# Optimization experiments

Hardware: AMD Instinct MI355X
Metric: run time of the kernel (lower is better)

The kernel has to match this reference:

```python
import jax, jax.numpy as jnp
import numpy as np

EMBED_DIM = 512
N_HEAD = 8
HEAD_DIM = EMBED_DIM // N_HEAD  # 64
B, S = 2, 4096
NEG_FILL = -1e20


def setup_inputs() -> dict:
    key = jax.random.key(0)
    ks = jax.random.split(key, 9)
    inp = {
        "key": jax.random.normal(ks[0], (B, S, EMBED_DIM), jnp.float32),
        "query": jax.random.normal(ks[1], (B, S, EMBED_DIM), jnp.float32),
        "value": jax.random.normal(ks[2], (B, S, EMBED_DIM), jnp.float32),
        "mask": jax.random.randint(ks[3], (1, 1, S, S), 0, 2, jnp.int32),
        # per-head projections (shared across heads, as in the source: a single
        # d x d nn.Linear applied to the last dim of [B,S,H,d])
        "Wq": jax.random.normal(ks[4], (HEAD_DIM, HEAD_DIM), jnp.float32) / np.sqrt(HEAD_DIM),
        "Wk": jax.random.normal(ks[5], (HEAD_DIM, HEAD_DIM), jnp.float32) / np.sqrt(HEAD_DIM),
        "Wv": jax.random.normal(ks[6], (HEAD_DIM, HEAD_DIM), jnp.float32) / np.sqrt(HEAD_DIM),
        "Wo": jax.random.normal(ks[7], (EMBED_DIM, EMBED_DIM), jnp.float32) / np.sqrt(EMBED_DIM),
        "bo": jax.random.normal(ks[8], (EMBED_DIM,), jnp.float32) * 0.01,
    }
    return inp


def reference(key, query, value, mask, Wq, Wk, Wv, Wo, bo):
    b, sq, e = query.shape
    skv = key.shape[1]
    h, d = N_HEAD, HEAD_DIM
    # split heads: [B, S, H, d]
    q = query.reshape(b, sq, h, d) @ Wq.T
    k = key.reshape(b, skv, h, d) @ Wk.T
    v = value.reshape(b, skv, h, d) @ Wv.T
    # scores: [B, H, Sq, Skv]
    scores = jnp.einsum("bqhd,bkhd->bhqk", q, k)
    # source masks BEFORE scaling: fill -1e20 then divide by sqrt(d)
    scores = jnp.where(mask == 0, NEG_FILL, scores)
    scores = scores / np.sqrt(d).astype(np.float32)
    attn = jax.nn.softmax(scores, axis=-1)
    ctx = jnp.einsum("bhqk,bkhd->bqhd", attn, v)  # [B, Sq, H, d]
    concat = ctx.reshape(b, sq, h * d)
    return concat @ Wo.T + bo
```

## Files before the change

### kernel.cpp

```cpp
#include <hip/hip_runtime.h>

typedef __bf16 bf16;
typedef __attribute__((ext_vector_type(8)))  bf16     bf16x8;
typedef __attribute__((ext_vector_type(4)))  bf16     bf16x4;
typedef __attribute__((ext_vector_type(16))) float    f32x16;
typedef __attribute__((ext_vector_type(4)))  float    f32x4;
typedef __attribute__((ext_vector_type(4)))  unsigned uint4v;
typedef __attribute__((ext_vector_type(2)))  unsigned uint2v;

#define SLEN 4096
#define HDIM 64
#define EMB 512
#define NTILES 64
#define SCALE_LOG2E 0.1803336100254854f

__device__ __forceinline__ f32x16 mfma32(bf16x8 a, bf16x8 b, f32x16 c) {
  return __builtin_amdgcn_mfma_f32_32x32x16_bf16(a, b, c, 0, 0, 0);
}

__device__ __forceinline__ void cp16(const void* g, const void* l) {
  __builtin_amdgcn_global_load_lds(
      (__attribute__((address_space(1))) unsigned int*)(unsigned long long)g,
      (__attribute__((address_space(3))) unsigned int*)(unsigned int)(unsigned long long)l,
      16, 0, 0);
}

__device__ __forceinline__ unsigned pk2(float a, float b) {
  unsigned short ua = __builtin_bit_cast(unsigned short, (bf16)a);
  unsigned short ub = __builtin_bit_cast(unsigned short, (bf16)b);
  return (unsigned)ua | ((unsigned)ub << 16);
}

__global__ __launch_bounds__(256, 2) void proj_qkv(
    const float* __restrict__ key, const float* __restrict__ query, const float* __restrict__ value,
    const float* __restrict__ Wq, const float* __restrict__ Wk, const float* __restrict__ Wv,
    bf16* __restrict__ Qb, bf16* __restrict__ Kb, bf16* __restrict__ VT)
{
  __shared__ __align__(16) bf16 tile[128][64];
  const int tid = threadIdx.x, w = tid >> 6, lane = tid & 63, l31 = lane & 31, lh = lane >> 5;
  const int r0 = blockIdx.x * 128;
  const int m0 = r0 + w * 32;

  #pragma unroll
  for (int p = 0; p < 3; ++p) {
    const float* X = (p == 0) ? query : (p == 1) ? key : value;
    const float* W = (p == 0) ? Wq    : (p == 1) ? Wk  : Wv;

    bf16x8 af[4];
    {
      const float* xr = X + (size_t)(m0 + l31) * 64 + 8 * lh;
      #pragma unroll
      for (int c = 0; c < 4; ++c) {
        f32x4 lo = *(const f32x4*)(xr + c * 16);
        f32x4 hi = *(const f32x4*)(xr + c * 16 + 4);
        bf16x8 v;
        #pragma unroll
        for (int j = 0; j < 4; ++j) { v[j] = (bf16)lo[j]; v[4 + j] = (bf16)hi[j]; }
        af[c] = v;
      }
    }
    bf16x8 bfr[2][4];
    #pragma unroll
    for (int nb = 0; nb < 2; ++nb) {
      const float* wr = W + (size_t)(l31 + 32 * nb) * 64 + 8 * lh;
      #pragma unroll
      for (int c = 0; c < 4; ++c) {
        f32x4 lo = *(const f32x4*)(wr + c * 16);
        f32x4 hi = *(const f32x4*)(wr + c * 16 + 4);
        bf16x8 v;
        #pragma unroll
        for (int j = 0; j < 4; ++j) { v[j] = (bf16)lo[j]; v[4 + j] = (bf16)hi[j]; }
        bfr[nb][c] = v;
      }
    }
    f32x16 a0, a1;
    #pragma unroll
    for (int r = 0; r < 16; ++r) { a0[r] = 0.f; a1[r] = 0.f; }
    #pragma unroll
    for (int c = 0; c < 4; ++c) {
      a0 = mfma32(af[c], bfr[0][c], a0);
      a1 = mfma32(af[c], bfr[1][c], a1);
    }

    const float qs = (p == 0) ? SCALE_LOG2E : 1.0f;
    __syncthreads();
    #pragma unroll
    for (int r = 0; r < 16; ++r) {
      const int row = w * 32 + (r & 3) + 8 * (r >> 2) + 4 * lh;
      tile[row][l31]      = (bf16)(a0[r] * qs);
      tile[row][l31 + 32] = (bf16)(a1[r] * qs);
    }
    __syncthreads();

    if (p < 2) {
      bf16* OUT = p ? Kb : Qb;
      const int rloc = tid >> 1, hf = tid & 1;
      const int rg = r0 + rloc, bs = rg >> 3, h = rg & 7, b = bs >> 12, sidx = bs & 4095;
      bf16* dst = OUT + (((size_t)(b * 8 + h) * SLEN + sidx) * 64 + hf * 32);
      const bf16* srcp = &tile[rloc][hf * 32];
      #pragma unroll
      for (int u = 0; u < 4; ++u) *(uint4v*)(dst + u * 8) = *(const uint4v*)(srcp + u * 8);
    } else {
      const int h = tid >> 5, d0 = tid & 31;
      const int b = blockIdx.x >> 8, s0 = (blockIdx.x * 16) & 4095;
      #pragma unroll
      for (int dh = 0; dh < 2; ++dh) {
        const int dd = d0 + 32 * dh;
        unsigned pk4[8];
        #pragma unroll
        for (int t2 = 0; t2 < 8; ++t2) {
          unsigned short ua = __builtin_bit_cast(unsigned short, tile[(2 * t2) * 8 + h][dd]);
          unsigned short ub = __builtin_bit_cast(unsigned short, tile[(2 * t2 + 1) * 8 + h][dd]);
          pk4[t2] = (unsigned)ua | ((unsigned)ub << 16);
        }
        bf16* dst = VT + ((size_t)(b * 8 + h) * 64 + dd) * SLEN + s0;
        uint4v A; A[0] = pk4[0]; A[1] = pk4[1]; A[2] = pk4[2]; A[3] = pk4[3];
        uint4v Bv; Bv[0] = pk4[4]; Bv[1] = pk4[5]; Bv[2] = pk4[6]; Bv[3] = pk4[7];
        *(uint4v*)(dst) = A;
        *(uint4v*)(dst + 8) = Bv;
      }
    }
  }
}

__device__ __forceinline__ unsigned nib_compress(unsigned x) {
  x = (x | (x >> 4)) & 0x00FF00FFu;
  x = (x | (x >> 8)) & 0x0000FFFFu;
  return x;
}
__global__ void pack_mask(const int* __restrict__ mask, unsigned* __restrict__ MW)
{
  const int w = threadIdx.x >> 6, lane = threadIdx.x & 63;
  const int q = blockIdx.x * 4 + w;
  const int* row = mask + (size_t)q * SLEN;
  unsigned long long mine = 0ull;
  #pragma unroll 4
  for (int i = 0; i < 64; ++i) {
    unsigned long long b = __ballot(row[i * 64 + lane] != 0);
    if (i == lane) mine = b;
  }
  const unsigned lo = (unsigned)mine, hi = (unsigned)(mine >> 32);
  const unsigned w0 = nib_compress(lo & 0x0F0F0F0Fu)        | (nib_compress(hi & 0x0F0F0F0Fu) << 16);
  const unsigned w1 = nib_compress((lo >> 4) & 0x0F0F0F0Fu) | (nib_compress((hi >> 4) & 0x0F0F0F0Fu) << 16);
  MW[(size_t)lane * SLEN + q] = w0;
  MW[(size_t)NTILES * SLEN + (size_t)lane * SLEN + q] = w1;
}

__global__ void wo_split(const float* __restrict__ Wo, bf16* __restrict__ WH, bf16* __restrict__ WL)
{
  const int i = (blockIdx.x * 256 + threadIdx.x) * 4;
  f32x4 v = *(const f32x4*)(Wo + i);
  bf16x4 h, l;
  #pragma unroll
  for (int j = 0; j < 4; ++j) { h[j] = (bf16)v[j]; l[j] = (bf16)(v[j] - (float)h[j]); }
  *(bf16x4*)(WH + i) = h;
  *(bf16x4*)(WL + i) = l;
}

__global__ __launch_bounds__(128, 4) void attn_kernel(
    const bf16* __restrict__ Qb, const bf16* __restrict__ Kb, const bf16* __restrict__ VT,
    const unsigned* __restrict__ MW,
    bf16* __restrict__ ctxh, bf16* __restrict__ ctxl)
{
  __shared__ __align__(16) unsigned char smem[16384];

  const int tid = threadIdx.x, w = tid >> 6, lane = tid & 63, l31 = lane & 31, lh = lane >> 5;
  const int logical = (blockIdx.x & 7) * 128 + (blockIdx.x >> 3);
  const int bh = logical >> 6, qt = logical & 63;
  const int q0w = qt * 64 + w * 32;
  const int qrow = q0w + l31;
  const int lh4 = 4 * lh;

  const bf16* qp = Qb + ((size_t)bh * SLEN + qrow) * HDIM + 8 * lh;
  const bf16x8 qf0 = *(const bf16x8*)(qp);
  const bf16x8 qf1 = *(const bf16x8*)(qp + 16);
  const bf16x8 qf2 = *(const bf16x8*)(qp + 32);
  const bf16x8 qf3 = *(const bf16x8*)(qp + 48);

  const bf16* kp0 = Kb + ((size_t)bh * SLEN + l31) * HDIM + (2 * w) * 16 + 8 * lh;
  const bf16* kp1 = kp0 + 16;
  const bf16* vp0 = VT + ((size_t)bh * HDIM + w * 32 + l31) * SLEN + 8 * lh;
  const bf16* vp1 = vp0 + 16;

  const int fk = 2 * w * 1024;
  const int fv = 4096 + 2 * w * 1024;
  const int lb = lane * 16;

  f32x16 o0, o1, Z16;
  #pragma unroll
  for (int r = 0; r < 16; ++r) { o0[r] = 0.f; o1[r] = 0.f; Z16[r] = 0.f; }
  float la0 = 0.f, la1 = 0.f, la2 = 0.f, la3 = 0.f;

#define STAGE(BUF) { \
  cp16(kp0, smem + (BUF) * 8192 + fk); cp16(kp1, smem + (BUF) * 8192 + fk + 1024); \
  cp16(vp0, smem + (BUF) * 8192 + fv); cp16(vp1, smem + (BUF) * 8192 + fv + 1024); \
  kp0 += 2048; kp1 += 2048; vp0 += 32; vp1 += 32; \
}

#define TILEC(BUF, MWORD, SH) { \
  const unsigned char* kr = smem + (BUF) * 8192 + lb; \
  __builtin_amdgcn_s_setprio(1); \
  f32x16 s = mfma32(*(const bf16x8*)(kr), qf0, Z16); \
  s = mfma32(*(const bf16x8*)(kr + 1024), qf1, s); \
  s = mfma32(*(const bf16x8*)(kr + 2048), qf2, s); \
  s = mfma32(*(const bf16x8*)(kr + 3072), qf3, s); \
  __builtin_amdgcn_s_setprio(0); \
  const unsigned mwk = (MWORD) >> (SH); \
  float p[16]; \
  _Pragma("unroll") \
  for (int r = 0; r < 16; ++r) { \
    float e = __builtin_amdgcn_exp2f(s[r]); \
    unsigned kbit = (unsigned)(((int)(mwk << (31 - r))) >> 31); \
    e = __builtin_bit_cast(float, __builtin_bit_cast(unsigned, e) & kbit); \
    p[r] = e; \
    if ((r & 3) == 0) la0 += e; else if ((r & 3) == 1) la1 += e; \
    else if ((r & 3) == 2) la2 += e; else la3 += e; \
  } \
  bf16x8 bp0, bp1; \
  { unsigned Wa = pk2(p[0], p[1]), Wb = pk2(p[2], p[3]); \
    unsigned Wc = pk2(p[4], p[5]), Wd = pk2(p[6], p[7]); \
    uint2v s02 = __builtin_amdgcn_permlane32_swap(Wa, Wc, false, false); \
    uint2v s13 = __builtin_amdgcn_permlane32_swap(Wb, Wd, false, false); \
    uint4v fw; fw[0] = s02[0]; fw[1] = s13[0]; fw[2] = s02[1]; fw[3] = s13[1]; \
    bp0 = __builtin_bit_cast(bf16x8, fw); } \
  { unsigned Wa = pk2(p[8], p[9]), Wb = pk2(p[10], p[11]); \
    unsigned Wc = pk2(p[12], p[13]), Wd = pk2(p[14], p[15]); \
    uint2v s02 = __builtin_amdgcn_permlane32_swap(Wa, Wc, false, false); \
    uint2v s13 = __builtin_amdgcn_permlane32_swap(Wb, Wd, false, false); \
    uint4v fw; fw[0] = s02[0]; fw[1] = s13[0]; fw[2] = s02[1]; fw[3] = s13[1]; \
    bp1 = __builtin_bit_cast(bf16x8, fw); } \
  const unsigned char* vr = kr + 4096; \
  __builtin_amdgcn_s_setprio(1); \
  o0 = mfma32(*(const bf16x8*)(vr), bp0, o0); \
  o0 = mfma32(*(const bf16x8*)(vr + 1024), bp1, o0); \
  o1 = mfma32(*(const bf16x8*)(vr + 2048), bp0, o1); \
  o1 = mfma32(*(const bf16x8*)(vr + 3072), bp1, o1); \
  __builtin_amdgcn_s_setprio(0); \
}

#define SYNC_STAGED \
  asm volatile("s_waitcnt vmcnt(4)" ::: "memory"); \
  __builtin_amdgcn_sched_barrier(0); \
  __builtin_amdgcn_s_barrier(); \
  __builtin_amdgcn_sched_barrier(0);

#define SYNC_READ_DONE \
  __builtin_amdgcn_sched_barrier(0); \
  __builtin_amdgcn_s_barrier(); \
  __builtin_amdgcn_sched_barrier(0);

  const unsigned* mp = MW + (size_t)lh * NTILES * SLEN + qrow;

  STAGE(0)
  unsigned mwc = *mp;

  for (int t2 = 0; t2 < 64; ++t2) {
    STAGE(1)
    SYNC_STAGED
    const unsigned mwn = mp[(t2 < 63) ? SLEN : 0];
    TILEC(0, mwc, 0)
    SYNC_READ_DONE

    STAGE(0)
    SYNC_STAGED
    TILEC(1, mwc, 16)
    SYNC_READ_DONE

    mwc = mwn; mp += SLEN;
  }
#undef STAGE
#undef TILEC
#undef SYNC_STAGED
#undef SYNC_READ_DONE

  asm volatile("s_waitcnt vmcnt(0)" ::: "memory");
  __builtin_amdgcn_s_barrier();

  float plsum = (la0 + la1) + (la2 + la3);
  plsum += __shfl_xor(plsum, 32);
  const float inv = 1.f / plsum;
  #pragma unroll
  for (int r = 0; r < 16; ++r) { o0[r] *= inv; o1[r] *= inv; }

  bf16* T = (bf16*)(smem + w * 8192);
  const int qq = lane >> 1, hf = lane & 1;
  bf16* dsth = ctxh + ((size_t)bh * SLEN + q0w + qq) * 64 + hf * 32;
  bf16* dstl = ctxl + ((size_t)bh * SLEN + q0w + qq) * 64 + hf * 32;
  const bf16* sp = T + qq * 72 + hf * 32;

  #pragma unroll
  for (int r = 0; r < 16; ++r) {
    const int dr = (r & 3) + 8 * (r >> 2) + lh4;
    T[l31 * 72 + dr]      = (bf16)o0[r];
    T[l31 * 72 + 32 + dr] = (bf16)o1[r];
  }
  #pragma unroll
  for (int u = 0; u < 4; ++u) *(uint4v*)(dsth + u * 8) = *(const uint4v*)(sp + u * 8);
  #pragma unroll
  for (int r = 0; r < 16; ++r) {
    const int dr = (r & 3) + 8 * (r >> 2) + lh4;
    const float h0 = (float)(bf16)o0[r];
    const float h1 = (float)(bf16)o1[r];
    T[l31 * 72 + dr]      = (bf16)(o0[r] - h0);
    T[l31 * 72 + 32 + dr] = (bf16)(o1[r] - h1);
  }
  #pragma unroll
  for (int u = 0; u < 4; ++u) *(uint4v*)(dstl + u * 8) = *(const uint4v*)(sp + u * 8);
}

__global__ __launch_bounds__(256, 2) void out_proj(
    const bf16* __restrict__ CH, const bf16* __restrict__ CL,
    const bf16* __restrict__ WH, const bf16* __restrict__ WL,
    const float* __restrict__ bo, float* __restrict__ out)
{
  __shared__ __align__(16) bf16 Af[2][4][4][64][8];
  const int tid = threadIdx.x, w = tid >> 6, lane = tid & 63, l31 = lane & 31, lh = lane >> 5;
  const int mt = blockIdx.x >> 3, nt = blockIdx.x & 7;
  const int bs0 = mt * 128, n0 = nt * 64;
  const int b = bs0 >> 12, sbase = bs0 & 4095;

  f32x16 a0, a1;
  #pragma unroll
  for (int r = 0; r < 16; ++r) { a0[r] = 0.f; a1[r] = 0.f; }

  for (int kk = 0; kk < 8; ++kk) {
    __syncthreads();
    #pragma unroll
    for (int qq = 0; qq < 8; ++qq) {
      const int fid = w * 8 + qq, pl = fid >> 4, mb = (fid >> 2) & 3, c = fid & 3;
      const bf16* src = (pl ? CL : CH) +
          ((size_t)(b * 8 + kk) * SLEN + sbase + 32 * mb + l31) * 64 + 16 * c + 8 * lh;
      cp16(src, &Af[pl][mb][c][0][0]);
    }
    __syncthreads();

    bf16x8 bh0[4], bl0[4], bh1[4], bl1[4], ah[4], al[4];
    #pragma unroll
    for (int c = 0; c < 4; ++c) {
      const size_t o0off = (size_t)(n0 + l31) * EMB + kk * 64 + 16 * c + 8 * lh;
      const size_t o1off = (size_t)(n0 + l31 + 32) * EMB + kk * 64 + 16 * c + 8 * lh;
      bh0[c] = *(const bf16x8*)(WH + o0off);
      bl0[c] = *(const bf16x8*)(WL + o0off);
      bh1[c] = *(const bf16x8*)(WH + o1off);
      bl1[c] = *(const bf16x8*)(WL + o1off);
      ah[c] = *(const bf16x8*)(&Af[0][w][c][lane][0]);
      al[c] = *(const bf16x8*)(&Af[1][w][c][lane][0]);
    }
    #pragma unroll
    for (int c = 0; c < 4; ++c) {
      a0 = mfma32(ah[c], bh0[c], a0);
      a0 = mfma32(ah[c], bl0[c], a0);
      a0 = mfma32(al[c], bh0[c], a0);
      a1 = mfma32(ah[c], bh1[c], a1);
      a1 = mfma32(ah[c], bl1[c], a1);
      a1 = mfma32(al[c], bh1[c], a1);
    }
  }

  const float bv0 = bo[n0 + l31], bv1 = bo[n0 + l31 + 32];
  #pragma unroll
  for (int r = 0; r < 16; ++r) {
    const int row = bs0 + w * 32 + (r & 3) + 8 * (r >> 2) + 4 * lh;
    out[(size_t)row * EMB + n0 + l31]      = a0[r] + bv0;
    out[(size_t)row * EMB + n0 + l31 + 32] = a1[r] + bv1;
  }
}

extern "C" void kernel_launch(void* const* d_in, const int* in_sizes, int n_in,
                              void* d_out, int out_size, void* d_ws, size_t ws_size,
                              hipStream_t stream)
{
  (void)in_sizes; (void)n_in; (void)out_size; (void)ws_size;
  const float* key   = (const float*)d_in[0];
  const float* query = (const float*)d_in[1];
  const float* value = (const float*)d_in[2];
  const int*   mask  = (const int*)d_in[3];
  const float* Wq    = (const float*)d_in[4];
  const float* Wk    = (const float*)d_in[5];
  const float* Wv    = (const float*)d_in[6];
  const float* Wo    = (const float*)d_in[7];
  const float* bo    = (const float*)d_in[8];
  float* out = (float*)d_out;

  char* ws = (char*)d_ws;
  bf16* Qb = (bf16*)(ws);
  bf16* Kb = (bf16*)(ws + (8ull  << 20));
  bf16* VT = (bf16*)(ws + (16ull << 20));
  unsigned* MW = (unsigned*)(ws + (24ull << 20));
  bf16* CH = (bf16*)(ws + (26ull << 20));
  bf16* CL = (bf16*)(ws + (34ull << 20));
  bf16* WH = (bf16*)(ws + (42ull << 20));
  bf16* WL = (bf16*)(ws + (42ull << 20) + (512ull << 10));

  proj_qkv<<<512, 256, 0, stream>>>(key, query, value, Wq, Wk, Wv, Qb, Kb, VT);
  pack_mask<<<1024, 256, 0, stream>>>(mask, MW);
  wo_split<<<256, 256, 0, stream>>>(Wo, WH, WL);
  attn_kernel<<<1024, 128, 0, stream>>>(Qb, Kb, VT, MW, CH, CL);
  out_proj<<<512, 256, 0, stream>>>(CH, CL, WH, WL, bo, out);
}
```

Before: 237.0 us.

## Split attention KV range into two halves and combine partial outputs

```diff
diff --git a/kernel.cpp b/kernel.cpp
--- a/kernel.cpp
+++ b/kernel.cpp
@@ -160,16 +160,16 @@
 __global__ __launch_bounds__(128, 4) void attn_kernel(
     const bf16* __restrict__ Qb, const bf16* __restrict__ Kb, const bf16* __restrict__ VT,
     const unsigned* __restrict__ MW,
-    bf16* __restrict__ ctxh, bf16* __restrict__ ctxl)
+    float* __restrict__ PO, float* __restrict__ PLg)
 {
   __shared__ __align__(16) unsigned char smem[16384];
 
   const int tid = threadIdx.x, w = tid >> 6, lane = tid & 63, l31 = lane & 31, lh = lane >> 5;
-  const int logical = (blockIdx.x & 7) * 128 + (blockIdx.x >> 3);
-  const int bh = logical >> 6, qt = logical & 63;
+  const int logical = (blockIdx.x & 7) * 256 + (blockIdx.x >> 3);
+  const int qt = logical & 63, bh = (logical >> 6) & 15, half = logical >> 10;
   const int q0w = qt * 64 + w * 32;
   const int qrow = q0w + l31;
-  const int lh4 = 4 * lh;
+  const int kv0 = half * 2048;
 
   const bf16* qp = Qb + ((size_t)bh * SLEN + qrow) * HDIM + 8 * lh;
   const bf16x8 qf0 = *(const bf16x8*)(qp);
@@ -177,9 +177,9 @@
   const bf16x8 qf2 = *(const bf16x8*)(qp + 32);
   const bf16x8 qf3 = *(const bf16x8*)(qp + 48);
 
-  const bf16* kp0 = Kb + ((size_t)bh * SLEN + l31) * HDIM + (2 * w) * 16 + 8 * lh;
+  const bf16* kp0 = Kb + ((size_t)bh * SLEN + kv0 + l31) * HDIM + (2 * w) * 16 + 8 * lh;
   const bf16* kp1 = kp0 + 16;
-  const bf16* vp0 = VT + ((size_t)bh * HDIM + w * 32 + l31) * SLEN + 8 * lh;
+  const bf16* vp0 = VT + ((size_t)bh * HDIM + w * 32 + l31) * SLEN + kv0 + 8 * lh;
   const bf16* vp1 = vp0 + 16;
 
   const int fk = 2 * w * 1024;
@@ -249,15 +249,15 @@
   __builtin_amdgcn_s_barrier(); \
   __builtin_amdgcn_sched_barrier(0);
 
-  const unsigned* mp = MW + (size_t)lh * NTILES * SLEN + qrow;
+  const unsigned* mp = MW + (size_t)lh * NTILES * SLEN + (size_t)(half * 32) * SLEN + qrow;
 
   STAGE(0)
   unsigned mwc = *mp;
 
-  for (int t2 = 0; t2 < 64; ++t2) {
+  for (int t2 = 0; t2 < 32; ++t2) {
     STAGE(1)
     SYNC_STAGED
-    const unsigned mwn = mp[(t2 < 63) ? SLEN : 0];
+    const unsigned mwn = mp[(t2 < 31) ? SLEN : 0];
     TILEC(0, mwc, 0)
     SYNC_READ_DONE
 
@@ -278,34 +278,66 @@
 
   float plsum = (la0 + la1) + (la2 + la3);
   plsum += __shfl_xor(plsum, 32);
-  const float inv = 1.f / plsum;
-  #pragma unroll
-  for (int r = 0; r < 16; ++r) { o0[r] *= inv; o1[r] *= inv; }
-
-  bf16* T = (bf16*)(smem + w * 8192);
-  const int qq = lane >> 1, hf = lane & 1;
-  bf16* dsth = ctxh + ((size_t)bh * SLEN + q0w + qq) * 64 + hf * 32;
-  bf16* dstl = ctxl + ((size_t)bh * SLEN + q0w + qq) * 64 + hf * 32;
-  const bf16* sp = T + qq * 72 + hf * 32;
+
+  float* T = (float*)(smem + w * 8192);
+  const int qq = lane >> 1, hx = lane & 1;
+  float* dst = PO + ((size_t)((half * 16 + bh) * SLEN + q0w + qq)) * 64 + hx * 16;
+  const float* sp = T + qq * 33 + hx * 16;
 
   #pragma unroll
   for (int r = 0; r < 16; ++r) {
-    const int dr = (r & 3) + 8 * (r >> 2) + lh4;
-    T[l31 * 72 + dr]      = (bf16)o0[r];
-    T[l31 * 72 + 32 + dr] = (bf16)o1[r];
-  }
-  #pragma unroll
-  for (int u = 0; u < 4; ++u) *(uint4v*)(dsth + u * 8) = *(const uint4v*)(sp + u * 8);
+    const int dr = (r & 3) + 8 * (r >> 2) + 4 * lh;
+    T[l31 * 33 + dr] = o0[r];
+  }
+  #pragma unroll
+  for (int u = 0; u < 4; ++u) *(f32x4*)(dst + u * 4) = *(const f32x4*)(sp + u * 4);
   #pragma unroll
   for (int r = 0; r < 16; ++r) {
-    const int dr = (r & 3) + 8 * (r >> 2) + lh4;
-    const float h0 = (float)(bf16)o0[r];
-    const float h1 = (float)(bf16)o1[r];
-    T[l31 * 72 + dr]      = (bf16)(o0[r] - h0);
-    T[l31 * 72 + 32 + dr] = (bf16)(o1[r] - h1);
-  }
-  #pragma unroll
-  for (int u = 0; u < 4; ++u) *(uint4v*)(dstl + u * 8) = *(const uint4v*)(sp + u * 8);
+    const int dr = (r & 3) + 8 * (r >> 2) + 4 * lh;
+    T[l31 * 33 + dr] = o1[r];
+  }
+  #pragma unroll
+  for (int u = 0; u < 4; ++u) *(f32x4*)(dst + 32 + u * 4) = *(const f32x4*)(sp + u * 4);
+
+  if (lane < 32) PLg[(size_t)(half * 16 + bh) * SLEN + q0w + l31] = plsum;
+}
+
+__global__ __launch_bounds__(256) void combine_halves(
+    const float* __restrict__ PO, const float* __restrict__ PLg,
+    bf16* __restrict__ CH, bf16* __restrict__ CL)
+{
+  const int bh = blockIdx.x >> 5, qt = blockIdx.x & 31;
+  const int t = threadIdx.x;
+  const int q = qt * 128 + (t >> 1);
+  const size_t HOFF = (size_t)16 * SLEN * 64;
+  const size_t base = ((size_t)bh * SLEN + q) * 64 + (t & 1) * 32;
+  const float inv = 1.f / (PLg[(size_t)bh * SLEN + q] +
+                           PLg[(size_t)16 * SLEN + (size_t)bh * SLEN + q]);
+  const float* p0 = PO + base;
+  const float* p1 = PO + HOFF + base;
+  unsigned hw[16], lw[16];
+  #pragma unroll
+  for (int i = 0; i < 8; ++i) {
+    f32x4 a = *(const f32x4*)(p0 + i * 4);
+    f32x4 b = *(const f32x4*)(p1 + i * 4);
+    float v0 = (a[0] + b[0]) * inv, v1 = (a[1] + b[1]) * inv;
+    float v2 = (a[2] + b[2]) * inv, v3 = (a[3] + b[3]) * inv;
+    float h0 = (float)(bf16)v0, h1 = (float)(bf16)v1;
+    float h2 = (float)(bf16)v2, h3 = (float)(bf16)v3;
+    hw[i * 2]     = pk2(v0, v1);
+    hw[i * 2 + 1] = pk2(v2, v3);
+    lw[i * 2]     = pk2(v0 - h0, v1 - h1);
+    lw[i * 2 + 1] = pk2(v2 - h2, v3 - h3);
+  }
+  bf16* ch = CH + base;
+  bf16* cl = CL + base;
+  #pragma unroll
+  for (int u = 0; u < 4; ++u) {
+    uint4v H; H[0] = hw[u*4]; H[1] = hw[u*4+1]; H[2] = hw[u*4+2]; H[3] = hw[u*4+3];
+    uint4v L; L[0] = lw[u*4]; L[1] = lw[u*4+1]; L[2] = lw[u*4+2]; L[3] = lw[u*4+3];
+    *(uint4v*)(ch + u * 8) = H;
+    *(uint4v*)(cl + u * 8) = L;
+  }
 }
 
 __global__ __launch_bounds__(256, 2) void out_proj(
@@ -391,10 +423,13 @@
   bf16* CL = (bf16*)(ws + (34ull << 20));
   bf16* WH = (bf16*)(ws + (42ull << 20));
   bf16* WL = (bf16*)(ws + (42ull << 20) + (512ull << 10));
+  float* PO  = (float*)(ws + (44ull << 20));
+  float* PLg = (float*)(ws + (78ull << 20));
 
   proj_qkv<<<512, 256, 0, stream>>>(key, query, value, Wq, Wk, Wv, Qb, Kb, VT);
   pack_mask<<<1024, 256, 0, stream>>>(mask, MW);
   wo_split<<<256, 256, 0, stream>>>(Wo, WH, WL);
-  attn_kernel<<<1024, 128, 0, stream>>>(Qb, Kb, VT, MW, CH, CL);
+  attn_kernel<<<2048, 128, 0, stream>>>(Qb, Kb, VT, MW, PO, PLg);
+  combine_halves<<<512, 256, 0, stream>>>(PO, PLg, CH, CL);
   out_proj<<<512, 256, 0, stream>>>(CH, CL, WH, WL, bo, out);
 }
```

After: 246.4 us. 1.04x slower.
